# Optimization experiments

Measured on AMD Instinct MI355X. Metric: run time of the kernel, lower is better.

The kernel has to match this reference:

```python
import jax, jax.numpy as jnp
import numpy as np

D_MODEL = 1024
N_HEADS = 16
D_K = D_MODEL // N_HEADS
BATCH = 2
SEQ = 2048


def setup_inputs() -> dict:
    key = jax.random.key(0)
    ks = jax.random.split(key, 9)
    s = 1.0 / np.sqrt(D_MODEL)
    x = jax.random.normal(ks[0], (BATCH, SEQ, D_MODEL), dtype=jnp.float32)
    # nn.Linear params: weight [out, in], bias [out]
    w_q = jax.random.uniform(ks[1], (D_MODEL, D_MODEL), jnp.float32, -s, s)
    b_q = jax.random.uniform(ks[2], (D_MODEL,), jnp.float32, -s, s)
    w_k = jax.random.uniform(ks[3], (D_MODEL, D_MODEL), jnp.float32, -s, s)
    b_k = jax.random.uniform(ks[4], (D_MODEL,), jnp.float32, -s, s)
    w_v = jax.random.uniform(ks[5], (D_MODEL, D_MODEL), jnp.float32, -s, s)
    b_v = jax.random.uniform(ks[6], (D_MODEL,), jnp.float32, -s, s)
    w_o = jax.random.uniform(ks[7], (D_MODEL, D_MODEL), jnp.float32, -s, s)
    b_o = jax.random.uniform(ks[8], (D_MODEL,), jnp.float32, -s, s)
    return {"x": x, "w_q": w_q, "b_q": b_q, "w_k": w_k, "b_k": b_k,
            "w_v": w_v, "b_v": b_v, "w_o": w_o, "b_o": b_o}


def reference(x, w_q, b_q, w_k, b_k, w_v, b_v, w_o, b_o):
    B, S, _ = x.shape
    # Linear projections, then split heads: [B, H, S, d_k]
    def proj(w, b):
        y = jnp.einsum('bsd,ed->bse', x, w) + b
        return y.reshape(B, S, N_HEADS, D_K).transpose(0, 2, 1, 3)
    q = proj(w_q, b_q)
    k = proj(w_k, b_k)
    v = proj(w_v, b_v)
    scores = jnp.einsum('bhqd,bhkd->bhqk', q, k) / jnp.sqrt(jnp.float32(D_K))
    attn = jax.nn.softmax(scores, axis=-1)  # dropout is identity in eval mode
    out = jnp.einsum('bhqk,bhkd->bhqd', attn, v)
    out = out.transpose(0, 2, 1, 3).reshape(B, S, D_MODEL)
    out = jnp.einsum('bsd,ed->bse', out, w_o) + b_o
    return out, attn
```

## Files before the change

kernel.cpp:

```cpp
#include <hip/hip_runtime.h>
#include <hip/hip_bf16.h>
#include <stdint.h>


typedef __attribute__((ext_vector_type(4))) float f32x4;
typedef __attribute__((ext_vector_type(8))) short s16x8;
typedef __attribute__((ext_vector_type(4))) unsigned short u16x4;

#define MFMA(a, b, c) __builtin_amdgcn_mfma_f32_16x16x32_bf16((a), (b), (c), 0, 0, 0)

__device__ __forceinline__ unsigned short f2bf(float f) {
    unsigned int u = __float_as_uint(f);
    unsigned int r = (u + 0x7FFFu + ((u >> 16) & 1u)) >> 16;
    return (unsigned short)r;
}

__global__ void convert_kernel(const float* __restrict__ x,
                               const float* __restrict__ wq, const float* __restrict__ wk,
                               const float* __restrict__ wv, const float* __restrict__ wo,
                               unsigned short* __restrict__ xb, unsigned short* __restrict__ wb) {
    size_t g = (size_t)blockIdx.x * blockDim.x + threadIdx.x;
    size_t i4 = g * 4;
    const float* src;
    unsigned short* dst;
    size_t off;
    if (i4 < 4194304) {
        src = x; dst = xb; off = i4;
    } else {
        size_t j = i4 - 4194304;
        int wsel = (int)(j >> 20);
        off = j & 1048575;
        src = (wsel == 0) ? wq : (wsel == 1) ? wk : (wsel == 2) ? wv : wo;
        dst = wb + ((size_t)wsel << 20);
    }
    float4 v = *(const float4*)(src + off);
    u16x4 o;
    o[0] = f2bf(v.x); o[1] = f2bf(v.y); o[2] = f2bf(v.z); o[3] = f2bf(v.w);
    *(u16x4*)(dst + off) = o;
}

__global__ __launch_bounds__(256, 2) void gemm_kernel(
    const unsigned short* __restrict__ A, const unsigned short* __restrict__ B,
    const float* __restrict__ bias_q, const float* __restrict__ bias_k,
    const float* __restrict__ bias_v, int mode,
    unsigned short* __restrict__ Qs, unsigned short* __restrict__ Kb,
    unsigned short* __restrict__ Vt, float* __restrict__ outp) {
    const int t = threadIdx.x;
    const int lane = t & 63;
    const int w = t >> 6;
    const int wr = w >> 1, wc = w & 1;
    const int rowbase = blockIdx.y * 128;
    const int colbase = blockIdx.x * 128;

    __shared__ unsigned short lA[2][128 * 40];
    __shared__ unsigned short lB[2][128 * 40];

    const int sr = t >> 2;
    const int sc = (t & 3) * 8;

    const unsigned short* gA0 = A + (size_t)(rowbase + sr) * 1024 + sc;
    const unsigned short* gA1 = A + (size_t)(rowbase + sr + 64) * 1024 + sc;
    const unsigned short* gB0 = B + (size_t)(colbase + sr) * 1024 + sc;
    const unsigned short* gB1 = B + (size_t)(colbase + sr + 64) * 1024 + sc;

    f32x4 acc[4][4];
#pragma unroll
    for (int mi = 0; mi < 4; ++mi)
#pragma unroll
        for (int ni = 0; ni < 4; ++ni)
            acc[mi][ni] = (f32x4){0.f, 0.f, 0.f, 0.f};

    uint4 va0 = *(const uint4*)(gA0);
    uint4 va1 = *(const uint4*)(gA1);
    uint4 vb0 = *(const uint4*)(gB0);
    uint4 vb1 = *(const uint4*)(gB1);
    *(uint4*)&lA[0][sr * 40 + sc] = va0;
    *(uint4*)&lA[0][(sr + 64) * 40 + sc] = va1;
    *(uint4*)&lB[0][sr * 40 + sc] = vb0;
    *(uint4*)&lB[0][(sr + 64) * 40 + sc] = vb1;
    __syncthreads();

    const int koff = (lane >> 4) * 8;
    const int ar = wr * 64 + (lane & 15);
    const int br = wc * 64 + (lane & 15);

    int cur = 0;
    for (int kt = 0; kt < 32; ++kt) {
        if (kt < 31) {
            int ko = (kt + 1) * 32;
            va0 = *(const uint4*)(gA0 + ko);
            va1 = *(const uint4*)(gA1 + ko);
            vb0 = *(const uint4*)(gB0 + ko);
            vb1 = *(const uint4*)(gB1 + ko);
        }
        s16x8 af[4], bf[4];
#pragma unroll
        for (int mi = 0; mi < 4; ++mi)
            af[mi] = *(const s16x8*)&lA[cur][(ar + mi * 16) * 40 + koff];
#pragma unroll
        for (int ni = 0; ni < 4; ++ni)
            bf[ni] = *(const s16x8*)&lB[cur][(br + ni * 16) * 40 + koff];
#pragma unroll
        for (int mi = 0; mi < 4; ++mi)
#pragma unroll
            for (int ni = 0; ni < 4; ++ni)
                acc[mi][ni] = MFMA(af[mi], bf[ni], acc[mi][ni]);
        if (kt < 31) {
            int nb = cur ^ 1;
            *(uint4*)&lA[nb][sr * 40 + sc] = va0;
            *(uint4*)&lA[nb][(sr + 64) * 40 + sc] = va1;
            *(uint4*)&lB[nb][sr * 40 + sc] = vb0;
            *(uint4*)&lB[nb][(sr + 64) * 40 + sc] = vb1;
        }
        __syncthreads();
        cur ^= 1;
    }

    if (mode == 1) {
#pragma unroll
        for (int ni = 0; ni < 4; ++ni) {
            int n = colbase + wc * 64 + ni * 16 + (lane & 15);
            float bv = bias_q[n];
#pragma unroll
            for (int mi = 0; mi < 4; ++mi) {
#pragma unroll
                for (int reg = 0; reg < 4; ++reg) {
                    int m = rowbase + wr * 64 + mi * 16 + (lane >> 4) * 4 + reg;
                    outp[(size_t)m * 1024 + n] = acc[mi][ni][reg] + bv;
                }
            }
        }
    } else {
        const int proj = colbase >> 10;
        const float* bias = (proj == 0) ? bias_q : (proj == 1) ? bias_k : bias_v;
        const float scale = (proj == 0) ? 0.18033688011112042f : 1.0f;
#pragma unroll
        for (int ni = 0; ni < 4; ++ni) {
            int n = colbase + wc * 64 + ni * 16 + (lane & 15);
            int nn = n & 1023;
            int h = nn >> 6, d = nn & 63;
            float bv = bias[nn];
#pragma unroll
            for (int mi = 0; mi < 4; ++mi) {
                int m0 = rowbase + wr * 64 + mi * 16 + (lane >> 4) * 4;
                int b = m0 >> 11, s0 = m0 & 2047;
                if (proj == 2) {
                    u16x4 pk;
#pragma unroll
                    for (int reg = 0; reg < 4; ++reg)
                        pk[reg] = f2bf(acc[mi][ni][reg] + bv);
                    *(u16x4*)&Vt[((size_t)(b * 16 + h) * 64 + d) * 2048 + s0] = pk;
                } else {
                    unsigned short* dstp = (proj == 0) ? Qs : Kb;
#pragma unroll
                    for (int reg = 0; reg < 4; ++reg)
                        dstp[((size_t)(b * 16 + h) * 2048 + (s0 + reg)) * 64 + d] =
                            f2bf((acc[mi][ni][reg] + bv) * scale);
                }
            }
        }
    }
}

__global__ __launch_bounds__(256, 2) void attn_kernel(
    const unsigned short* __restrict__ Qs, const unsigned short* __restrict__ Kb,
    const unsigned short* __restrict__ Vt, float* __restrict__ attn,
    unsigned short* __restrict__ ctx) {
    const int t = threadIdx.x;
    const int lane = t & 63;
    const int l15 = lane & 15;
    const int g = lane >> 4;
    const int g4 = g * 4, g8 = g * 8;
    const int w = t >> 6;
    const int wr = w >> 1, wc = w & 1;
    const int qt = blockIdx.x;
    const int bh = blockIdx.y;
    const int b = bh >> 4, h = bh & 15;

    const unsigned short* Qh = Qs + (size_t)bh * (2048 * 64);
    const unsigned short* Kh = Kb + (size_t)bh * (2048 * 64);
    const unsigned short* Vh = Vt + (size_t)bh * (64 * 2048);
    float* attn_h = attn + (size_t)bh * (2048 * 2048) + (size_t)(qt * 128) * 2048;

    __shared__ unsigned short lP[2][128 * 72];
    __shared__ float lred[2][128];

    s16x8 qf[8];
#pragma unroll
    for (int mi = 0; mi < 4; ++mi)
#pragma unroll
        for (int kk = 0; kk < 2; ++kk)
            qf[mi * 2 + kk] =
                *(const s16x8*)&Qh[(size_t)(qt * 128 + wr * 64 + mi * 16 + l15) * 64 + kk * 32 + g8];

    s16x8 kf0[4], kf1[4], vf0[4], vf1[4];

#define K_LOAD(DST, KT)                                                                     \
    {                                                                                       \
        _Pragma("unroll") for (int ni = 0; ni < 2; ++ni)                                    \
            _Pragma("unroll") for (int kk = 0; kk < 2; ++kk)                                \
                DST[ni * 2 + kk] = *(const s16x8*)&Kh[(size_t)((KT) * 64 + wc * 32 +        \
                                                               ni * 16 + l15) * 64 +        \
                                                      kk * 32 + g8];                        \
    }
#define V_LOAD(DST, KT)                                                                     \
    {                                                                                       \
        _Pragma("unroll") for (int ni = 0; ni < 2; ++ni)                                    \
            _Pragma("unroll") for (int ks = 0; ks < 2; ++ks)                                \
                DST[ni * 2 + ks] = *(const s16x8*)&Vh[(size_t)(wc * 32 + ni * 16 + l15) *   \
                                                          2048 +                            \
                                                      (KT) * 64 + ks * 32 + g8];            \
    }
#define QK_MFMA(KF, SACC)                                                                   \
    {                                                                                       \
        _Pragma("unroll") for (int kk = 0; kk < 2; ++kk)                                    \
            _Pragma("unroll") for (int mi = 0; mi < 4; ++mi)                                \
                _Pragma("unroll") for (int ni = 0; ni < 2; ++ni)                            \
                    SACC[mi][ni] = MFMA(KF[ni * 2 + kk], qf[mi * 2 + kk], SACC[mi][ni]);    \
    }

    float qsum[4] = {0.f, 0.f, 0.f, 0.f};
    K_LOAD(kf0, 0);
#define P1_BODY(KF, KFN, KT)                                                                \
    {                                                                                       \
        f32x4 sacc[4][2];                                                                   \
        _Pragma("unroll") for (int mi = 0; mi < 4; ++mi)                                    \
            _Pragma("unroll") for (int ni = 0; ni < 2; ++ni)                                \
                sacc[mi][ni] = (f32x4){0.f, 0.f, 0.f, 0.f};                                 \
        QK_MFMA(KF, sacc);                                                                  \
        if ((KT) < 31) K_LOAD(KFN, (KT) + 1);                                               \
        _Pragma("unroll") for (int mi = 0; mi < 4; ++mi) {                                  \
            float e = 0.f;                                                                  \
            _Pragma("unroll") for (int ni = 0; ni < 2; ++ni)                                \
                _Pragma("unroll") for (int r = 0; r < 4; ++r)                               \
                    e += exp2f(sacc[mi][ni][r]);                                            \
            qsum[mi] += e;                                                                  \
        }                                                                                   \
    }
    for (int k2 = 0; k2 < 16; ++k2) {
        P1_BODY(kf0, kf1, 2 * k2);
        P1_BODY(kf1, kf0, 2 * k2 + 1);
    }
#pragma unroll
    for (int mi = 0; mi < 4; ++mi) {
        float v = qsum[mi];
        v += __shfl_xor(v, 16);
        v += __shfl_xor(v, 32);
        qsum[mi] = v;
    }
    if (lane < 16) {
#pragma unroll
        for (int mi = 0; mi < 4; ++mi)
            lred[wc][wr * 64 + mi * 16 + lane] = qsum[mi];
    }
    __syncthreads();
    float rl[4];
#pragma unroll
    for (int mi = 0; mi < 4; ++mi) {
        int q = wr * 64 + mi * 16 + l15;
        rl[mi] = 1.0f / (lred[0][q] + lred[1][q]);
    }

    f32x4 oacc[4][2];
#pragma unroll
    for (int mi = 0; mi < 4; ++mi)
#pragma unroll
        for (int ni = 0; ni < 2; ++ni) oacc[mi][ni] = (f32x4){0.f, 0.f, 0.f, 0.f};

    K_LOAD(kf0, 0);
    V_LOAD(vf0, 0);
#define P2_BODY(BUF, KF, KFN, VF, VFN, KT)                                                  \
    {                                                                                       \
        f32x4 sacc[4][2];                                                                   \
        _Pragma("unroll") for (int mi = 0; mi < 4; ++mi)                                    \
            _Pragma("unroll") for (int ni = 0; ni < 2; ++ni)                                \
                sacc[mi][ni] = (f32x4){0.f, 0.f, 0.f, 0.f};                                 \
        QK_MFMA(KF, sacc);                                                                  \
        if ((KT) < 31) {                                                                    \
            K_LOAD(KFN, (KT) + 1);                                                          \
            V_LOAD(VFN, (KT) + 1);                                                          \
        }                                                                                   \
        _Pragma("unroll") for (int mi = 0; mi < 4; ++mi) {                                  \
            const int q = wr * 64 + mi * 16 + l15;                                          \
            _Pragma("unroll") for (int ni = 0; ni < 2; ++ni) {                              \
                float4 pv;                                                                  \
                pv.x = exp2f(sacc[mi][ni][0]) * rl[mi];                                     \
                pv.y = exp2f(sacc[mi][ni][1]) * rl[mi];                                     \
                pv.z = exp2f(sacc[mi][ni][2]) * rl[mi];                                     \
                pv.w = exp2f(sacc[mi][ni][3]) * rl[mi];                                     \
                *(float4*)&attn_h[(size_t)q * 2048 + (KT) * 64 + wc * 32 + ni * 16 + g4] =  \
                    pv;                                                                     \
                u16x4 pk;                                                                   \
                pk[0] = f2bf(pv.x);                                                         \
                pk[1] = f2bf(pv.y);                                                         \
                pk[2] = f2bf(pv.z);                                                         \
                pk[3] = f2bf(pv.w);                                                         \
                *(u16x4*)&lP[BUF][q * 72 + wc * 32 + ni * 16 + g4] = pk;                    \
            }                                                                               \
        }                                                                                   \
        __syncthreads();                                                                    \
        _Pragma("unroll") for (int ks = 0; ks < 2; ++ks) {                                  \
            s16x8 pf[4];                                                                    \
            _Pragma("unroll") for (int mi = 0; mi < 4; ++mi)                                \
                pf[mi] =                                                                    \
                    *(const s16x8*)&lP[BUF][(wr * 64 + mi * 16 + l15) * 72 + ks * 32 + g8]; \
            _Pragma("unroll") for (int mi = 0; mi < 4; ++mi)                                \
                _Pragma("unroll") for (int ni = 0; ni < 2; ++ni)                            \
                    oacc[mi][ni] = MFMA(pf[mi], VF[ni * 2 + ks], oacc[mi][ni]);             \
        }                                                                                   \
    }
    for (int k2 = 0; k2 < 16; ++k2) {
        P2_BODY(0, kf0, kf1, vf0, vf1, 2 * k2);
        P2_BODY(1, kf1, kf0, vf1, vf0, 2 * k2 + 1);
    }

#pragma unroll
    for (int mi = 0; mi < 4; ++mi) {
#pragma unroll
        for (int ni = 0; ni < 2; ++ni) {
            int d = wc * 32 + ni * 16 + l15;
#pragma unroll
            for (int r = 0; r < 4; ++r) {
                int q = qt * 128 + wr * 64 + mi * 16 + g4 + r;
                ctx[((size_t)(b * 2048 + q)) * 1024 + h * 64 + d] = f2bf(oacc[mi][ni][r]);
            }
        }
    }
#undef K_LOAD
#undef V_LOAD
#undef QK_MFMA
#undef P1_BODY
#undef P2_BODY
}

extern "C" void kernel_launch(void* const* d_in, const int* in_sizes, int n_in,
                              void* d_out, int out_size, void* d_ws, size_t ws_size,
                              hipStream_t stream) {
    const float* x  = (const float*)d_in[0];
    const float* wq = (const float*)d_in[1];
    const float* bq = (const float*)d_in[2];
    const float* wk = (const float*)d_in[3];
    const float* bk = (const float*)d_in[4];
    const float* wv = (const float*)d_in[5];
    const float* bv = (const float*)d_in[6];
    const float* wo = (const float*)d_in[7];
    const float* bo = (const float*)d_in[8];

    char* ws = (char*)d_ws;
    unsigned short* xb  = (unsigned short*)(ws);
    unsigned short* wb  = (unsigned short*)(ws + 8388608);
    unsigned short* Qsc = (unsigned short*)(ws + 16777216);
    unsigned short* Kb  = (unsigned short*)(ws + 25165824);
    unsigned short* Vt  = (unsigned short*)(ws + 33554432);
    unsigned short* ctx = (unsigned short*)(ws + 41943040);

    float* out  = (float*)d_out;
    float* attn = out + 4194304;

    convert_kernel<<<8192, 256, 0, stream>>>(x, wq, wk, wv, wo, xb, wb);
    gemm_kernel<<<dim3(24, 32), 256, 0, stream>>>(xb, wb, bq, bk, bv, 0,
                                                  Qsc, Kb, Vt, nullptr);
    attn_kernel<<<dim3(16, 32), 256, 0, stream>>>(Qsc, Kb, Vt, attn, ctx);
    gemm_kernel<<<dim3(8, 32), 256, 0, stream>>>(ctx, wb + 3 * 1048576, bo, bo, bo, 1,
                                                 nullptr, nullptr, nullptr, out);
}
```

Measured before the change: 277.4 us.

## Load GEMM tiles directly to LDS with global_load_lds and larger K-tile

Replaces the register-staged double-buffered LDS load in the projection GEMM with direct global-to-LDS loads (global_load_lds), a single LDS buffer, and a K-tile of 64 instead of 32. Launch bounds are raised to 3 blocks per CU. The aim is to cut VGPR use and the register round trip, halve the number of barrier-separated iterations, and raise occupancy. In exchange it drops the overlap of global loads with MFMA work and removes the row padding, so the unpadded 64-wide rows may cause LDS bank conflicts on the fragment reads.

Measured after the change: 279.2 us. Within noise of the previous version (+0.7%).

```diff
diff --git a/kernel.cpp b/kernel.cpp
--- a/kernel.cpp
+++ b/kernel.cpp
@@ -39,7 +39,7 @@
     *(u16x4*)(dst + off) = o;
 }
 
-__global__ __launch_bounds__(256, 2) void gemm_kernel(
+__global__ __launch_bounds__(256, 3) void gemm_kernel(
     const unsigned short* __restrict__ A, const unsigned short* __restrict__ B,
     const float* __restrict__ bias_q, const float* __restrict__ bias_k,
     const float* __restrict__ bias_v, int mode,
@@ -47,21 +47,16 @@
     unsigned short* __restrict__ Vt, float* __restrict__ outp) {
     const int t = threadIdx.x;
     const int lane = t & 63;
-    const int w = t >> 6;
-    const int wr = w >> 1, wc = w & 1;
+    const int wv4 = t >> 6;
+    const int wr = wv4 >> 1, wc = wv4 & 1;
     const int rowbase = blockIdx.y * 128;
     const int colbase = blockIdx.x * 128;
 
-    __shared__ unsigned short lA[2][128 * 40];
-    __shared__ unsigned short lB[2][128 * 40];
-
-    const int sr = t >> 2;
-    const int sc = (t & 3) * 8;
-
-    const unsigned short* gA0 = A + (size_t)(rowbase + sr) * 1024 + sc;
-    const unsigned short* gA1 = A + (size_t)(rowbase + sr + 64) * 1024 + sc;
-    const unsigned short* gB0 = B + (size_t)(colbase + sr) * 1024 + sc;
-    const unsigned short* gB1 = B + (size_t)(colbase + sr + 64) * 1024 + sc;
+    __shared__ __align__(16) unsigned short lA[128 * 64];
+    __shared__ __align__(16) unsigned short lB[128 * 64];
+
+    const int crow = lane >> 3;
+    const int ccol = (lane & 7) * 8;
 
     f32x4 acc[4][4];
 #pragma unroll
@@ -70,56 +65,47 @@
         for (int ni = 0; ni < 4; ++ni)
             acc[mi][ni] = (f32x4){0.f, 0.f, 0.f, 0.f};
 
-    uint4 va0 = *(const uint4*)(gA0);
-    uint4 va1 = *(const uint4*)(gA1);
-    uint4 vb0 = *(const uint4*)(gB0);
-    uint4 vb1 = *(const uint4*)(gB1);
-    *(uint4*)&lA[0][sr * 40 + sc] = va0;
-    *(uint4*)&lA[0][(sr + 64) * 40 + sc] = va1;
-    *(uint4*)&lB[0][sr * 40 + sc] = vb0;
-    *(uint4*)&lB[0][(sr + 64) * 40 + sc] = vb1;
-    __syncthreads();
-
+    const int l15 = lane & 15;
     const int koff = (lane >> 4) * 8;
-    const int ar = wr * 64 + (lane & 15);
-    const int br = wc * 64 + (lane & 15);
-
-    int cur = 0;
-    for (int kt = 0; kt < 32; ++kt) {
-        if (kt < 31) {
-            int ko = (kt + 1) * 32;
-            va0 = *(const uint4*)(gA0 + ko);
-            va1 = *(const uint4*)(gA1 + ko);
-            vb0 = *(const uint4*)(gB0 + ko);
-            vb1 = *(const uint4*)(gB1 + ko);
-        }
-        s16x8 af[4], bf[4];
-#pragma unroll
-        for (int mi = 0; mi < 4; ++mi)
-            af[mi] = *(const s16x8*)&lA[cur][(ar + mi * 16) * 40 + koff];
-#pragma unroll
-        for (int ni = 0; ni < 4; ++ni)
-            bf[ni] = *(const s16x8*)&lB[cur][(br + ni * 16) * 40 + koff];
-#pragma unroll
-        for (int mi = 0; mi < 4; ++mi)
+    const int ar = wr * 64 + l15;
+    const int br = wc * 64 + l15;
+
+    for (int kt = 0; kt < 16; ++kt) {
+        const int kbase = kt * 64 + ccol;
+#pragma unroll
+        for (int i = 0; i < 4; ++i) {
+            const int c = wv4 * 4 + i;
+            const int r = c * 8 + crow;
+            __builtin_amdgcn_global_load_lds(
+                (const __attribute__((address_space(1))) void*)(A + (size_t)(rowbase + r) * 1024 + kbase),
+                (__attribute__((address_space(3))) void*)&lA[c * 512], 16, 0, 0);
+            __builtin_amdgcn_global_load_lds(
+                (const __attribute__((address_space(1))) void*)(B + (size_t)(colbase + r) * 1024 + kbase),
+                (__attribute__((address_space(3))) void*)&lB[c * 512], 16, 0, 0);
+        }
+        __syncthreads();
+#pragma unroll
+        for (int kk = 0; kk < 2; ++kk) {
+            s16x8 af[4], bf[4];
+#pragma unroll
+            for (int mi = 0; mi < 4; ++mi)
+                af[mi] = *(const s16x8*)&lA[(ar + mi * 16) * 64 + kk * 32 + koff];
 #pragma unroll
             for (int ni = 0; ni < 4; ++ni)
-                acc[mi][ni] = MFMA(af[mi], bf[ni], acc[mi][ni]);
-        if (kt < 31) {
-            int nb = cur ^ 1;
-            *(uint4*)&lA[nb][sr * 40 + sc] = va0;
-            *(uint4*)&lA[nb][(sr + 64) * 40 + sc] = va1;
-            *(uint4*)&lB[nb][sr * 40 + sc] = vb0;
-            *(uint4*)&lB[nb][(sr + 64) * 40 + sc] = vb1;
+                bf[ni] = *(const s16x8*)&lB[(br + ni * 16) * 64 + kk * 32 + koff];
+#pragma unroll
+            for (int mi = 0; mi < 4; ++mi)
+#pragma unroll
+                for (int ni = 0; ni < 4; ++ni)
+                    acc[mi][ni] = MFMA(af[mi], bf[ni], acc[mi][ni]);
         }
         __syncthreads();
-        cur ^= 1;
     }
 
     if (mode == 1) {
 #pragma unroll
         for (int ni = 0; ni < 4; ++ni) {
-            int n = colbase + wc * 64 + ni * 16 + (lane & 15);
+            int n = colbase + wc * 64 + ni * 16 + l15;
             float bv = bias_q[n];
 #pragma unroll
             for (int mi = 0; mi < 4; ++mi) {
@@ -136,7 +122,7 @@
         const float scale = (proj == 0) ? 0.18033688011112042f : 1.0f;
 #pragma unroll
         for (int ni = 0; ni < 4; ++ni) {
-            int n = colbase + wc * 64 + ni * 16 + (lane & 15);
+            int n = colbase + wc * 64 + ni * 16 + l15;
             int nn = n & 1023;
             int h = nn >> 6, d = nn & 63;
             float bv = bias[nn];
```
